# Performance work log

Measured on AMD Instinct MI355X. Metric: run time of the kernel, lower is better.

Reference implementation:

```python
import jax, jax.numpy as jnp
import numpy as np

B, VMAX, EGO, H, ACT = 2048, 128, 15, 256, 2


def _u(k, shape, fan):
    s = 1.0 / np.sqrt(fan)
    return jax.random.uniform(k, shape, jnp.float32, -s, s)


def setup_inputs() -> dict:
    key = jax.random.key(0)
    ks = jax.random.split(key, 20)
    return {
        "state": jax.random.normal(ks[0], (B, VMAX, EGO), jnp.float32),
        "lengths": jax.random.randint(ks[1], (B,), 1, VMAX + 1),
        "Wih1": _u(ks[2], (4 * H, EGO), H), "Whh1": _u(ks[3], (4 * H, H), H),
        "bih1": _u(ks[4], (4 * H,), H), "bhh1": _u(ks[5], (4 * H,), H),
        "W1": _u(ks[6], (1024, H), H), "b1": _u(ks[7], (1024,), H),
        "W2": _u(ks[8], (1024, 1024), 1024), "b2": _u(ks[9], (1024,), 1024),
        "W3": _u(ks[10], (512, 1024), 1024), "b3": _u(ks[11], (512,), 1024),
        "W4": _u(ks[12], (256, 512), 512), "b4": _u(ks[13], (256,), 512),
        "Wih2": _u(ks[14], (4 * H, H), H), "Whh2": _u(ks[15], (4 * H, H), H),
        "bih2": _u(ks[16], (4 * H,), H), "bhh2": _u(ks[17], (4 * H,), H),
        "Wpi": _u(ks[18], (ACT, H), H), "bpi": _u(ks[19], (ACT,), H),
    }


def lstm_cell(x, h, c, Wih, Whh, bih, bhh):
    # torch.nn.LSTMCell: gates ordered i, f, g, o
    g = x @ Wih.T + bih + h @ Whh.T + bhh  # [B, 4H]
    i, f, gg, o = jnp.split(g, 4, axis=-1)
    c = jax.nn.sigmoid(f) * c + jax.nn.sigmoid(i) * jnp.tanh(gg)
    h = jax.nn.sigmoid(o) * jnp.tanh(c)
    return h, c


def reference(state, lengths, Wih1, Whh1, bih1, bhh1, W1, b1, W2, b2,
              W3, b3, W4, b4, Wih2, Whh2, bih2, bhh2, Wpi, bpi):
    Bn, V, _ = state.shape
    z = jnp.zeros((Bn, H), state.dtype)

    # Encoder: per-vehicle LSTM over ragged lengths (masked updates).
    def enc_step(carry, xs):
        h, c = carry
        x_t, t = xs
        hn, cn = lstm_cell(x_t, h, c, Wih1, Whh1, bih1, bhh1)
        m = (t < lengths)[:, None]
        return (jnp.where(m, hn, h), jnp.where(m, cn, c)), None
    (h, _), _ = jax.lax.scan(enc_step, (z, z),
                             (state.transpose(1, 0, 2), jnp.arange(V)))

    x = jax.nn.relu(h @ W1.T + b1)
    x = jax.nn.relu(x @ W2.T + b2)
    x = jax.nn.relu(x @ W3.T + b3)
    x = jax.nn.relu(x @ W4.T + b4)  # [B, 256]

    # Decoder: repeats the SAME input x each step; action = tanh(pi(cx))
    # (original applies pi to the cell state cx, kept faithful).
    def dec_step(carry, _):
        h, c = carry
        hn, cn = lstm_cell(x, h, c, Wih2, Whh2, bih2, bhh2)
        act = jnp.tanh(cn @ Wpi.T + bpi)
        return (hn, cn), act
    _, acts = jax.lax.scan(dec_step, (z, z), None, length=V)  # [V, B, ACT]
    acts = acts.transpose(1, 0, 2)  # [B, V, ACT]

    # Zero out padded timesteps (ragged output represented as padded dense).
    mask = (jnp.arange(V)[None, :] < lengths[:, None])[..., None]
    return acts * mask.astype(acts.dtype)
```

## Files before the change

### kernel.cpp

```cpp
#include <hip/hip_runtime.h>

typedef _Float16 f16;
typedef _Float16 f16x8 __attribute__((ext_vector_type(8)));
typedef float f32x4 __attribute__((ext_vector_type(4)));

#define MFMA(a,b,c) __builtin_amdgcn_mfma_f32_16x16x32_f16(a,b,c,0,0,0)

constexpr int B_ = 2048, V_ = 128, EGO_ = 15, H_ = 256;
constexpr int MT = 16;
constexpr int ENC_KT = 9;
constexpr int DEC_KT = 8;
constexpr int HSTR = 296;
constexpr int DSTR = 264;


__device__ __forceinline__ float sigf(float x){ return 1.f/(1.f+__expf(-x)); }
__device__ __forceinline__ float tanh_fast(float x){ return 1.f - 2.f/(1.f+__expf(2.f*x)); }
__device__ __forceinline__ void pin(f16x8& v){ asm volatile("" : "+v"(v)); }

__device__ __forceinline__ void st_u32(uint32_t* p, uint32_t v){
    __hip_atomic_store(p, v, __ATOMIC_RELAXED, __HIP_MEMORY_SCOPE_AGENT);
}
__device__ __forceinline__ uint32_t ld_u32(const uint32_t* p){
    return __hip_atomic_load(p, __ATOMIC_RELAXED, __HIP_MEMORY_SCOPE_AGENT);
}
union cvt8 { f16x8 h; uint32_t u[4]; };

__global__ void prepack_enc(const float* __restrict__ Whh1, const float* __restrict__ Wih1,
                            f16* __restrict__ dst){
    int id = blockIdx.x*256 + threadIdx.x;
    if (id >= 2*4*8*ENC_KT*64) return;
    int L = id & 63; int c = id >> 6;
    int kt = c % ENC_KT; c /= ENC_KT;
    int nt = c & 7; c >>= 3;
    int w = c & 3; int hb = c >> 2;
    int n = (nt>>1)*256 + hb*128 + w*32 + (nt&1)*16 + (L&15);
    int kbase = kt*32 + (L>>4)*8;
    #pragma unroll
    for (int j=0;j<8;++j){
        int k = kbase + j;
        float x = (k < 256) ? Whh1[n*256 + k] : ((k < 271) ? Wih1[n*15 + (k-256)] : 0.f);
        dst[(size_t)id*8 + j] = (f16)x;
    }
}
__global__ void prepack_dec(const float* __restrict__ Whh2, f16* __restrict__ dst){
    int id = blockIdx.x*256 + threadIdx.x;
    if (id >= 2*4*8*DEC_KT*64) return;
    int L = id & 63; int c = id >> 6;
    int kt = c % DEC_KT; c /= DEC_KT;
    int nt = c & 7; c >>= 3;
    int w = c & 3; int hb = c >> 2;
    int n = (nt>>1)*256 + hb*128 + w*32 + (nt&1)*16 + (L&15);
    int kbase = kt*32 + (L>>4)*8;
    #pragma unroll
    for (int j=0;j<8;++j) dst[(size_t)id*8 + j] = (f16)Whh2[n*256 + kbase + j];
}
__global__ void bias_kernel(const float* bih1,const float* bhh1,const float* bih2,
                            const float* bhh2,float* be,float* bd){
    int i = blockIdx.x*256 + threadIdx.x;
    if (i < 1024){ be[i]=bih1[i]+bhh1[i]; bd[i]=bih2[i]+bhh2[i]; }
}
__global__ void convert_kernel(const float* __restrict__ src, f16* __restrict__ dst, int n){
    int i = blockIdx.x*256 + threadIdx.x;
    if (i < n) dst[i] = (f16)src[i];
}

__global__ __launch_bounds__(256,1) void encoder_kernel(
    const float* __restrict__ state, const int* __restrict__ lengths,
    const f16* __restrict__ Wp, const float* __restrict__ bias,
    f16* __restrict__ henc, f16* __restrict__ ebuf, int* __restrict__ flags)
{
    __shared__ __align__(16) f16 hcat[MT*HSTR];
    const int tid = threadIdx.x;
    const int wave = tid>>6, lane = tid&63, lr = lane&15, quad = lane>>4;
    const int bid = blockIdx.x, hb = bid>>7, g = bid&127, pbid = bid^128;
    const int row0 = g*MT;
    const int xr = tid>>4, xc = tid&15;

    for (int i=tid;i<MT*HSTR;i+=256) hcat[i] = (f16)0.f;

    int len_r[4];
    #pragma unroll
    for (int r=0;r<4;++r) len_r[r] = lengths[row0 + quad*4 + r];

    float bias_v[8];
    #pragma unroll
    for (int nt=0;nt<8;++nt)
        bias_v[nt] = bias[(nt>>1)*256 + hb*128 + wave*32 + (nt&1)*16 + lr];

    const f16x8* Wb = (const f16x8*)Wp + (size_t)((hb*4+wave)*8*ENC_KT)*64;
    f16x8 wreg[8][ENC_KT];
    #pragma unroll
    for (int nt=0;nt<8;++nt)
        #pragma unroll
        for (int kt=0;kt<ENC_KT;++kt){
            wreg[nt][kt] = Wb[(nt*ENC_KT + kt)*64 + lane];
            pin(wreg[nt][kt]);
        }

    float c_reg[8], h_reg[8];
    #pragma unroll
    for (int i=0;i<8;++i){ c_reg[i]=0.f; h_reg[i]=0.f; }

    __syncthreads();

    for (int t=0;t<V_;++t){
        if (tid < 240){
            int rr = tid/15, cc = tid - rr*15;
            hcat[rr*HSTR + 256 + cc] = (f16)state[(size_t)(row0+rr)*V_*EGO_ + t*EGO_ + cc];
        }
        __syncthreads();
        f32x4 acc[8];
        #pragma unroll
        for (int nt=0;nt<8;++nt) acc[nt] = (f32x4){bias_v[nt],bias_v[nt],bias_v[nt],bias_v[nt]};
        #pragma unroll
        for (int kt=0;kt<ENC_KT;++kt){
            f16x8 a = *(const f16x8*)&hcat[lr*HSTR + kt*32 + quad*8];
            #pragma unroll
            for (int nt=0;nt<8;++nt) acc[nt] = MFMA(a, wreg[nt][kt], acc[nt]);
        }
        __syncthreads();
        #pragma unroll
        for (int s=0;s<2;++s){
            #pragma unroll
            for (int r=0;r<4;++r){
                int idx = s*4 + r;
                float gi = acc[s][r],   gf = acc[2+s][r];
                float gg = acc[4+s][r], go = acc[6+s][r];
                float cn = sigf(gf)*c_reg[idx] + sigf(gi)*tanh_fast(gg);
                float hn = sigf(go)*tanh_fast(cn);
                bool upd = (t < len_r[r]);
                c_reg[idx] = upd ? cn : c_reg[idx];
                h_reg[idx] = upd ? hn : h_reg[idx];
                hcat[(quad*4+r)*HSTR + hb*128 + wave*32 + s*16 + lr] = (f16)h_reg[idx];
            }
        }
        __syncthreads();
        {
            cvt8 cv; cv.h = *(const f16x8*)&hcat[xr*HSTR + hb*128 + xc*8];
            uint32_t* dst = (uint32_t*)(ebuf + ((size_t)(t&1)*256 + bid)*2048) + xr*64 + xc*4;
            st_u32(dst+0,cv.u[0]); st_u32(dst+1,cv.u[1]);
            st_u32(dst+2,cv.u[2]); st_u32(dst+3,cv.u[3]);
        }
        __syncthreads();
        if (tid == 0){
            st_u32((uint32_t*)&flags[bid], (uint32_t)(t+1));
            while (ld_u32((const uint32_t*)&flags[pbid]) < (uint32_t)(t+1))
                __builtin_amdgcn_s_sleep(2);
        }
        __syncthreads();
        {
            const uint32_t* src = (const uint32_t*)(ebuf + ((size_t)(t&1)*256 + pbid)*2048) + xr*64 + xc*4;
            cvt8 cv;
            cv.u[0]=ld_u32(src+0); cv.u[1]=ld_u32(src+1);
            cv.u[2]=ld_u32(src+2); cv.u[3]=ld_u32(src+3);
            *(f16x8*)&hcat[xr*HSTR + (1-hb)*128 + xc*8] = cv.h;
        }
    }
    #pragma unroll
    for (int s=0;s<2;++s)
        #pragma unroll
        for (int r=0;r<4;++r)
            henc[(size_t)(row0+quad*4+r)*H_ + hb*128 + wave*32 + s*16 + lr] = (f16)h_reg[s*4+r];
}

template<bool RELU, bool F32OUT>
__global__ __launch_bounds__(256,2) void gemm_kernel(
    const f16* __restrict__ A, const f16* __restrict__ W,
    const float* __restrict__ bias, void* __restrict__ outp,
    int M, int N, int K)
{
    constexpr int ASTR = 40;
    __shared__ __align__(16) f16 As[64*ASTR];
    __shared__ __align__(16) f16 Ws[64*ASTR];
    const int tid = threadIdx.x;
    const int wave = tid>>6, lane = tid&63, lr = lane&15, quad = lane>>4;
    const int n0 = blockIdx.x*64, m0 = blockIdx.y*64;
    const int lrow = tid>>2, lk8 = (tid&3)*8;

    f32x4 acc[4];
    #pragma unroll
    for (int mt=0;mt<4;++mt) acc[mt] = (f32x4){0.f,0.f,0.f,0.f};

    for (int k0=0;k0<K;k0+=32){
        __syncthreads();
        *(f16x8*)&As[lrow*ASTR + lk8] = *(const f16x8*)&A[(size_t)(m0+lrow)*K + k0 + lk8];
        *(f16x8*)&Ws[lrow*ASTR + lk8] = *(const f16x8*)&W[(size_t)(n0+lrow)*K + k0 + lk8];
        __syncthreads();
        f16x8 b = *(const f16x8*)&Ws[(wave*16+lr)*ASTR + quad*8];
        #pragma unroll
        for (int mt=0;mt<4;++mt){
            f16x8 a = *(const f16x8*)&As[(mt*16+lr)*ASTR + quad*8];
            acc[mt] = MFMA(a, b, acc[mt]);
        }
    }
    float bv = bias[n0 + wave*16 + lr];
    #pragma unroll
    for (int mt=0;mt<4;++mt){
        #pragma unroll
        for (int r=0;r<4;++r){
            float v = acc[mt][r] + bv;
            if (RELU) v = fmaxf(v, 0.f);
            int m = m0 + mt*16 + quad*4 + r, n = n0 + wave*16 + lr;
            if (F32OUT) ((float*)outp)[(size_t)m*N + n] = v;
            else        ((f16*)outp)[(size_t)m*N + n] = (f16)v;
        }
    }
}

__global__ __launch_bounds__(256,1) void decoder_kernel(
    const int* __restrict__ lengths, const f16* __restrict__ Wp,
    const float* __restrict__ xdec, const float* __restrict__ Wpi,
    const float* __restrict__ bpi, float* __restrict__ out,
    f16* __restrict__ ebuf, int* __restrict__ flags, float* __restrict__ pbuf)
{
    __shared__ __align__(16) f16 hbuf[MT*DSTR];
    __shared__ float part[4][16][2];
    const int tid = threadIdx.x;
    const int wave = tid>>6, lane = tid&63, lr = lane&15, quad = lane>>4;
    const int bid = blockIdx.x, hb = bid>>7, g = bid&127, pbid = bid^128;
    const int row0 = g*MT;
    const int xr = tid>>4, xc = tid&15;

    for (int i=tid;i<MT*DSTR;i+=256) hbuf[i] = (f16)0.f;

    float xd[8][4];
    #pragma unroll
    for (int nt=0;nt<8;++nt){
        int n = (nt>>1)*256 + hb*128 + wave*32 + (nt&1)*16 + lr;
        #pragma unroll
        for (int r=0;r<4;++r) xd[nt][r] = xdec[(size_t)(row0+quad*4+r)*1024 + n];
    }
    float wpi_reg[2][2];
    #pragma unroll
    for (int a=0;a<2;++a)
        #pragma unroll
        for (int s=0;s<2;++s)
            wpi_reg[a][s] = Wpi[a*H_ + hb*128 + wave*32 + s*16 + lr];

    const f16x8* Wb = (const f16x8*)Wp + (size_t)((hb*4+wave)*8*DEC_KT)*64;
    f16x8 wreg[8][DEC_KT];
    #pragma unroll
    for (int nt=0;nt<8;++nt)
        #pragma unroll
        for (int kt=0;kt<DEC_KT;++kt){
            wreg[nt][kt] = Wb[(nt*DEC_KT + kt)*64 + lane];
            pin(wreg[nt][kt]);
        }

    float c_reg[8];
    #pragma unroll
    for (int i=0;i<8;++i) c_reg[i]=0.f;

    const int m_o = (tid>>1)&15, a_o = tid&1;
    const float bpi_o = bpi[a_o];
    const int len_o = (tid<32) ? lengths[row0+m_o] : 0;
    const size_t outbase = (size_t)(row0+m_o)*V_*2 + a_o;

    for (int t=0;t<V_;++t){
        __syncthreads();
        f32x4 acc[8];
        #pragma unroll
        for (int nt=0;nt<8;++nt) acc[nt] = (f32x4){xd[nt][0],xd[nt][1],xd[nt][2],xd[nt][3]};
        #pragma unroll
        for (int kt=0;kt<DEC_KT;++kt){
            f16x8 a = *(const f16x8*)&hbuf[lr*DSTR + kt*32 + quad*8];
            #pragma unroll
            for (int nt=0;nt<8;++nt) acc[nt] = MFMA(a, wreg[nt][kt], acc[nt]);
        }
        __syncthreads();
        float spi[4][2];
        #pragma unroll
        for (int r=0;r<4;++r){ spi[r][0]=0.f; spi[r][1]=0.f; }
        #pragma unroll
        for (int s=0;s<2;++s){
            #pragma unroll
            for (int r=0;r<4;++r){
                int idx = s*4 + r;
                float gi = acc[s][r],   gf = acc[2+s][r];
                float gg = acc[4+s][r], go = acc[6+s][r];
                float cn = sigf(gf)*c_reg[idx] + sigf(gi)*tanh_fast(gg);
                c_reg[idx] = cn;
                float hn = sigf(go)*tanh_fast(cn);
                hbuf[(quad*4+r)*DSTR + hb*128 + wave*32 + s*16 + lr] = (f16)hn;
                spi[r][0] += cn*wpi_reg[0][s];
                spi[r][1] += cn*wpi_reg[1][s];
            }
        }
        #pragma unroll
        for (int msk=1; msk<16; msk<<=1){
            #pragma unroll
            for (int r=0;r<4;++r){
                spi[r][0] += __shfl_xor(spi[r][0], msk, 64);
                spi[r][1] += __shfl_xor(spi[r][1], msk, 64);
            }
        }
        if (lr == 0){
            #pragma unroll
            for (int r=0;r<4;++r){
                part[wave][quad*4+r][0] = spi[r][0];
                part[wave][quad*4+r][1] = spi[r][1];
            }
        }
        __syncthreads();
        {
            cvt8 cv; cv.h = *(const f16x8*)&hbuf[xr*DSTR + hb*128 + xc*8];
            uint32_t* dst = (uint32_t*)(ebuf + ((size_t)(t&1)*256 + bid)*2048) + xr*64 + xc*4;
            st_u32(dst+0,cv.u[0]); st_u32(dst+1,cv.u[1]);
            st_u32(dst+2,cv.u[2]); st_u32(dst+3,cv.u[3]);
        }
        if (hb == 1 && tid < 32){
            float v = part[0][m_o][a_o]+part[1][m_o][a_o]+part[2][m_o][a_o]+part[3][m_o][a_o];
            st_u32((uint32_t*)pbuf + ((size_t)(t&1)*128 + g)*32 + tid, __float_as_uint(v));
        }
        __syncthreads();
        if (tid == 0){
            st_u32((uint32_t*)&flags[bid], (uint32_t)(t+1));
            while (ld_u32((const uint32_t*)&flags[pbid]) < (uint32_t)(t+1))
                __builtin_amdgcn_s_sleep(2);
        }
        __syncthreads();
        {
            const uint32_t* src = (const uint32_t*)(ebuf + ((size_t)(t&1)*256 + pbid)*2048) + xr*64 + xc*4;
            cvt8 cv;
            cv.u[0]=ld_u32(src+0); cv.u[1]=ld_u32(src+1);
            cv.u[2]=ld_u32(src+2); cv.u[3]=ld_u32(src+3);
            *(f16x8*)&hbuf[xr*DSTR + (1-hb)*128 + xc*8] = cv.h;
        }
        if (hb == 0 && tid < 32){
            uint32_t pu = ld_u32((const uint32_t*)pbuf + ((size_t)(t&1)*128 + g)*32 + tid);
            float v = part[0][m_o][a_o] + part[1][m_o][a_o]
                    + part[2][m_o][a_o] + part[3][m_o][a_o]
                    + __uint_as_float(pu) + bpi_o;
            v = tanh_fast(v);
            out[outbase + (size_t)t*2] = (t < len_o) ? v : 0.f;
        }
    }
}

extern "C" void kernel_launch(void* const* d_in, const int* in_sizes, int n_in,
                              void* d_out, int out_size, void* d_ws, size_t ws_size,
                              hipStream_t stream) {
    const float* state = (const float*)d_in[0];
    const int*   lengths=(const int*)d_in[1];
    const float* Wih1 = (const float*)d_in[2];
    const float* Whh1 = (const float*)d_in[3];
    const float* bih1 = (const float*)d_in[4];
    const float* bhh1 = (const float*)d_in[5];
    const float* W1   = (const float*)d_in[6];  const float* b1 = (const float*)d_in[7];
    const float* W2   = (const float*)d_in[8];  const float* b2 = (const float*)d_in[9];
    const float* W3   = (const float*)d_in[10]; const float* b3 = (const float*)d_in[11];
    const float* W4   = (const float*)d_in[12]; const float* b4 = (const float*)d_in[13];
    const float* Wih2 = (const float*)d_in[14]; const float* Whh2=(const float*)d_in[15];
    const float* bih2 = (const float*)d_in[16]; const float* bhh2=(const float*)d_in[17];
    const float* Wpi  = (const float*)d_in[18]; const float* bpi =(const float*)d_in[19];
    float* out = (float*)d_out;

    char* p = (char*)d_ws;
    auto alloc = [&](size_t bytes){ char* r = p; p += (bytes + 255) & ~(size_t)255; return r; };
    f16* WencP   = (f16*)alloc((size_t)2*4*8*ENC_KT*64*8*2);
    f16* WdecP   = (f16*)alloc((size_t)2*4*8*DEC_KT*64*8*2);
    f16* W1f     = (f16*)alloc((size_t)1024*256*2);
    f16* W2f     = (f16*)alloc((size_t)1024*1024*2);
    f16* W3f     = (f16*)alloc((size_t)512*1024*2);
    f16* W4f     = (f16*)alloc((size_t)256*512*2);
    f16* Wih2f   = (f16*)alloc((size_t)1024*256*2);
    float* biasE = (float*)alloc(1024*4);
    float* biasD = (float*)alloc(1024*4);
    f16* henc    = (f16*)alloc((size_t)2048*256*2);
    f16* act1    = (f16*)alloc((size_t)2048*1024*2);
    f16* act2    = (f16*)alloc((size_t)2048*1024*2);
    f16* act3    = (f16*)alloc((size_t)2048*512*2);
    f16* x4      = (f16*)alloc((size_t)2048*256*2);
    float* xdec  = (float*)alloc((size_t)2048*1024*4);
    f16* ebuf    = (f16*)alloc((size_t)2*256*2048*2);
    float* pbuf  = (float*)alloc((size_t)2*128*32*4);
    int* flags   = (int*)alloc((size_t)512*4);

    hipMemsetAsync(flags, 0, 512*4, stream);

    prepack_enc<<<(2*4*8*ENC_KT*64+255)/256,256,0,stream>>>(Whh1, Wih1, WencP);
    prepack_dec<<<(2*4*8*DEC_KT*64+255)/256,256,0,stream>>>(Whh2, WdecP);
    bias_kernel<<<4,256,0,stream>>>(bih1,bhh1,bih2,bhh2,biasE,biasD);
    convert_kernel<<<(1024*256+255)/256,256,0,stream>>>(W1, W1f, 1024*256);
    convert_kernel<<<(1024*1024+255)/256,256,0,stream>>>(W2, W2f, 1024*1024);
    convert_kernel<<<(512*1024+255)/256,256,0,stream>>>(W3, W3f, 512*1024);
    convert_kernel<<<(256*512+255)/256,256,0,stream>>>(W4, W4f, 256*512);
    convert_kernel<<<(1024*256+255)/256,256,0,stream>>>(Wih2, Wih2f, 1024*256);

    encoder_kernel<<<256,256,0,stream>>>(state, lengths, WencP, biasE, henc, ebuf, flags);

    gemm_kernel<true ,false><<<dim3(16,32),256,0,stream>>>(henc, W1f, b1, act1, 2048,1024,256);
    gemm_kernel<true ,false><<<dim3(16,32),256,0,stream>>>(act1, W2f, b2, act2, 2048,1024,1024);
    gemm_kernel<true ,false><<<dim3( 8,32),256,0,stream>>>(act2, W3f, b3, act3, 2048, 512,1024);
    gemm_kernel<true ,false><<<dim3( 4,32),256,0,stream>>>(act3, W4f, b4, x4,   2048, 256, 512);
    gemm_kernel<false,true ><<<dim3(16,32),256,0,stream>>>(x4, Wih2f, biasD, xdec, 2048,1024,256);

    decoder_kernel<<<256,256,0,stream>>>(lengths, WdecP, xdec, Wpi, bpi, out,
                                         ebuf, flags+256, pbuf);
}
```

Measured before the change: 1.438 ms.

## Feed partner hidden state from global straight into MFMA and drop per-step barriers

In both the encoder and decoder LSTM loops, the partner block's half of the hidden state is now loaded from the exchange buffer directly into registers and used as the MFMA A-operand, instead of first being copied into LDS. All threads wait on the partner flag at the start of the next step, not at the end of the current one, which removes two block barriers and an LDS round-trip per timestep. The encoder also prefetches the next timestep's input into a register, and the decoder defers the action output write by one step, with a final flush after the loop. The cost is that every thread now polls the flag and issues global loads on the critical path, which raises memory traffic.

```diff
diff --git a/kernel.cpp b/kernel.cpp
--- a/kernel.cpp
+++ b/kernel.cpp
@@ -102,22 +102,58 @@
     #pragma unroll
     for (int i=0;i<8;++i){ c_reg[i]=0.f; h_reg[i]=0.f; }
 
+    const bool sv = (tid < 240);
+    const int srr = tid/15, scc = tid - srr*15;
+    float xreg = sv ? state[(size_t)(row0+srr)*V_*EGO_ + 0*EGO_ + scc] : 0.f;
+
     __syncthreads();
 
     for (int t=0;t<V_;++t){
-        if (tid < 240){
-            int rr = tid/15, cc = tid - rr*15;
-            hcat[rr*HSTR + 256 + cc] = (f16)state[(size_t)(row0+rr)*V_*EGO_ + t*EGO_ + cc];
-        }
-        __syncthreads();
+        if (sv) hcat[srr*HSTR + 256 + scc] = (f16)xreg;
+        __syncthreads();
+        float xnext = (sv && t+1 < V_)
+            ? state[(size_t)(row0+srr)*V_*EGO_ + (t+1)*EGO_ + scc] : 0.f;
+
+        if (t > 0){
+            while (ld_u32((const uint32_t*)&flags[pbid]) < (uint32_t)t)
+                __builtin_amdgcn_s_sleep(1);
+        }
+        asm volatile("" ::: "memory");
+        cvt8 pa[4];
+        if (t > 0){
+            const uint32_t* ebp = (const uint32_t*)(ebuf + ((size_t)((t-1)&1)*256 + pbid)*2048);
+            #pragma unroll
+            for (int pkt=0;pkt<4;++pkt)
+                #pragma unroll
+                for (int i=0;i<4;++i)
+                    pa[pkt].u[i] = ld_u32(ebp + lr*64 + pkt*16 + quad*4 + i);
+        } else {
+            #pragma unroll
+            for (int pkt=0;pkt<4;++pkt)
+                #pragma unroll
+                for (int i=0;i<4;++i) pa[pkt].u[i] = 0u;
+        }
+
         f32x4 acc[8];
         #pragma unroll
         for (int nt=0;nt<8;++nt) acc[nt] = (f32x4){bias_v[nt],bias_v[nt],bias_v[nt],bias_v[nt]};
         #pragma unroll
-        for (int kt=0;kt<ENC_KT;++kt){
+        for (int k2=0;k2<4;++k2){
+            int kt = hb*4 + k2;
             f16x8 a = *(const f16x8*)&hcat[lr*HSTR + kt*32 + quad*8];
             #pragma unroll
             for (int nt=0;nt<8;++nt) acc[nt] = MFMA(a, wreg[nt][kt], acc[nt]);
+        }
+        {
+            f16x8 a = *(const f16x8*)&hcat[lr*HSTR + 8*32 + quad*8];
+            #pragma unroll
+            for (int nt=0;nt<8;++nt) acc[nt] = MFMA(a, wreg[nt][8], acc[nt]);
+        }
+        #pragma unroll
+        for (int pkt=0;pkt<4;++pkt){
+            int kt = (1-hb)*4 + pkt;
+            #pragma unroll
+            for (int nt=0;nt<8;++nt) acc[nt] = MFMA(pa[pkt].h, wreg[nt][kt], acc[nt]);
         }
         __syncthreads();
         #pragma unroll
@@ -143,19 +179,9 @@
             st_u32(dst+2,cv.u[2]); st_u32(dst+3,cv.u[3]);
         }
         __syncthreads();
-        if (tid == 0){
+        if (tid == 0)
             st_u32((uint32_t*)&flags[bid], (uint32_t)(t+1));
-            while (ld_u32((const uint32_t*)&flags[pbid]) < (uint32_t)(t+1))
-                __builtin_amdgcn_s_sleep(2);
-        }
-        __syncthreads();
-        {
-            const uint32_t* src = (const uint32_t*)(ebuf + ((size_t)(t&1)*256 + pbid)*2048) + xr*64 + xc*4;
-            cvt8 cv;
-            cv.u[0]=ld_u32(src+0); cv.u[1]=ld_u32(src+1);
-            cv.u[2]=ld_u32(src+2); cv.u[3]=ld_u32(src+3);
-            *(f16x8*)&hcat[xr*HSTR + (1-hb)*128 + xc*8] = cv.h;
-        }
+        xreg = xnext;
     }
     #pragma unroll
     for (int s=0;s<2;++s)
@@ -257,16 +283,52 @@
     const int len_o = (tid<32) ? lengths[row0+m_o] : 0;
     const size_t outbase = (size_t)(row0+m_o)*V_*2 + a_o;
 
+    __syncthreads();
+
     for (int t=0;t<V_;++t){
-        __syncthreads();
+        if (t > 0){
+            while (ld_u32((const uint32_t*)&flags[pbid]) < (uint32_t)t)
+                __builtin_amdgcn_s_sleep(1);
+        }
+        asm volatile("" ::: "memory");
+        if (t > 0 && hb == 0 && tid < 32){
+            uint32_t pu = ld_u32((const uint32_t*)pbuf + ((size_t)((t-1)&1)*128 + g)*32 + tid);
+            float v = part[0][m_o][a_o] + part[1][m_o][a_o]
+                    + part[2][m_o][a_o] + part[3][m_o][a_o]
+                    + __uint_as_float(pu) + bpi_o;
+            v = tanh_fast(v);
+            out[outbase + (size_t)(t-1)*2] = ((t-1) < len_o) ? v : 0.f;
+        }
+        cvt8 pa[4];
+        if (t > 0){
+            const uint32_t* ebp = (const uint32_t*)(ebuf + ((size_t)((t-1)&1)*256 + pbid)*2048);
+            #pragma unroll
+            for (int pkt=0;pkt<4;++pkt)
+                #pragma unroll
+                for (int i=0;i<4;++i)
+                    pa[pkt].u[i] = ld_u32(ebp + lr*64 + pkt*16 + quad*4 + i);
+        } else {
+            #pragma unroll
+            for (int pkt=0;pkt<4;++pkt)
+                #pragma unroll
+                for (int i=0;i<4;++i) pa[pkt].u[i] = 0u;
+        }
+
         f32x4 acc[8];
         #pragma unroll
         for (int nt=0;nt<8;++nt) acc[nt] = (f32x4){xd[nt][0],xd[nt][1],xd[nt][2],xd[nt][3]};
         #pragma unroll
-        for (int kt=0;kt<DEC_KT;++kt){
+        for (int k2=0;k2<4;++k2){
+            int kt = hb*4 + k2;
             f16x8 a = *(const f16x8*)&hbuf[lr*DSTR + kt*32 + quad*8];
             #pragma unroll
             for (int nt=0;nt<8;++nt) acc[nt] = MFMA(a, wreg[nt][kt], acc[nt]);
+        }
+        #pragma unroll
+        for (int pkt=0;pkt<4;++pkt){
+            int kt = (1-hb)*4 + pkt;
+            #pragma unroll
+            for (int nt=0;nt<8;++nt) acc[nt] = MFMA(pa[pkt].h, wreg[nt][kt], acc[nt]);
         }
         __syncthreads();
         float spi[4][2];
@@ -314,26 +376,20 @@
             st_u32((uint32_t*)pbuf + ((size_t)(t&1)*128 + g)*32 + tid, __float_as_uint(v));
         }
         __syncthreads();
-        if (tid == 0){
+        if (tid == 0)
             st_u32((uint32_t*)&flags[bid], (uint32_t)(t+1));
-            while (ld_u32((const uint32_t*)&flags[pbid]) < (uint32_t)(t+1))
-                __builtin_amdgcn_s_sleep(2);
-        }
-        __syncthreads();
-        {
-            const uint32_t* src = (const uint32_t*)(ebuf + ((size_t)(t&1)*256 + pbid)*2048) + xr*64 + xc*4;
-            cvt8 cv;
-            cv.u[0]=ld_u32(src+0); cv.u[1]=ld_u32(src+1);
-            cv.u[2]=ld_u32(src+2); cv.u[3]=ld_u32(src+3);
-            *(f16x8*)&hbuf[xr*DSTR + (1-hb)*128 + xc*8] = cv.h;
-        }
-        if (hb == 0 && tid < 32){
-            uint32_t pu = ld_u32((const uint32_t*)pbuf + ((size_t)(t&1)*128 + g)*32 + tid);
+    }
+    if (hb == 0){
+        while (ld_u32((const uint32_t*)&flags[pbid]) < (uint32_t)V_)
+            __builtin_amdgcn_s_sleep(1);
+        asm volatile("" ::: "memory");
+        if (tid < 32){
+            uint32_t pu = ld_u32((const uint32_t*)pbuf + ((size_t)((V_-1)&1)*128 + g)*32 + tid);
             float v = part[0][m_o][a_o] + part[1][m_o][a_o]
                     + part[2][m_o][a_o] + part[3][m_o][a_o]
                     + __uint_as_float(pu) + bpi_o;
             v = tanh_fast(v);
-            out[outbase + (size_t)t*2] = (t < len_o) ? v : 0.f;
+            out[outbase + (size_t)(V_-1)*2] = ((V_-1) < len_o) ? v : 0.f;
         }
     }
 }
```

Result: slower. 5.135 ms (+257.0%).
